# Kernel tuning notes

Hardware: AMD Instinct MI355X
Metric: run time of the kernel (lower is better)

The kernel has to match this reference:

```python
import jax, jax.numpy as jnp
import numpy as np

N_HEAD = 16
R = 4  # reciprocal rank

def setup_inputs() -> dict:
    key = jax.random.key(0)
    ks = jax.random.split(key, 8)
    B, T, C = 2, 2048, 1024
    H = N_HEAD
    D = C // H
    D_std = D - R
    x = jax.random.normal(ks[0], (B, T, C), dtype=jnp.float32)
    W_attn = jax.random.normal(ks[1], (3 * C, C), dtype=jnp.float32) * (1.0 / np.sqrt(C))
    W_proj = jax.random.normal(ks[2], (C, C), dtype=jnp.float32) * (1.0 / np.sqrt(C))
    w_std = jnp.full((H,), D_std / D, dtype=jnp.float32)
    w_rec = jnp.full((H,), R / D, dtype=jnp.float32)
    skip_std = jnp.float32(2.0)
    skip_low = jnp.float32(-3.0)
    rwr_alpha = jnp.full((H,), 0.05, dtype=jnp.float32)
    return {"x": x, "W_attn": W_attn, "W_proj": W_proj, "w_std": w_std,
            "w_rec": w_rec, "skip_std": skip_std, "skip_low": skip_low,
            "rwr_alpha": rwr_alpha}

def reference(x, W_attn, W_proj, w_std, w_rec, skip_std, skip_low, rwr_alpha):
    B, T, C = x.shape
    H = N_HEAD
    D = C // H
    D_std = D - R
    # fused QKV projection: [Qf | Kf | V]
    fused = jnp.einsum('btc,fc->btf', x, W_attn)
    qf, kf, v = jnp.split(fused, 3, axis=-1)
    Qf = qf.reshape(B, T, H, D).transpose(0, 2, 1, 3)  # (B,H,T,D)
    Kf = kf.reshape(B, T, H, D).transpose(0, 2, 1, 3)
    V = v.reshape(B, T, H, D).transpose(0, 2, 1, 3)
    # dynamic per-head gate scaling folded into Qf/Kf
    g_std = jnp.sqrt(jnp.clip(w_std * jax.nn.sigmoid(skip_std), 1e-8))  # (H,)
    g_rec = jnp.sqrt(jnp.clip(w_rec * jax.nn.sigmoid(skip_low), 1e-8))  # (H,)
    scale = jnp.concatenate([
        jnp.broadcast_to(g_std[:, None], (H, D_std)),
        jnp.broadcast_to(g_rec[:, None], (H, R)),
    ], axis=-1)  # (H, D)
    scale = scale[None, :, None, :]  # (1,H,1,D)
    Qf = Qf * scale
    Kf = Kf * scale
    # causal SDPA (scale = 1/sqrt(head_dim), dropout=0)
    scores = jnp.einsum('bhqd,bhkd->bhqk', Qf, Kf) / jnp.sqrt(jnp.float32(D))
    causal = jnp.tril(jnp.ones((T, T), dtype=bool))
    scores = jnp.where(causal[None, None], scores, jnp.float32(-1e30))
    attn = jax.nn.softmax(scores, axis=-1)
    y = jnp.einsum('bhqk,bhkd->bhqd', attn, V)
    # self-restart mix: out = (1-alpha)*attn_out + alpha*V, alpha in [0, 0.5]
    alpha = jnp.clip(rwr_alpha, 0.0, 0.5)[None, :, None, None]
    y = (1.0 - alpha) * y + alpha * V
    y = y.transpose(0, 2, 1, 3).reshape(B, T, C)
    return jnp.einsum('btc,oc->bto', y, W_proj)
```

## Files before the change

kernel.cpp:

```cpp
#include <hip/hip_runtime.h>
#include <hip/hip_bf16.h>
#include <math.h>
#include <stdint.h>

#define B_    2
#define T_    2048
#define C_    1024
#define H_    16
#define D_    64
#define R_    4
#define DSTD  60
#define F_    3072
#define BT_   (B_ * T_)

#define LOG2E 1.44269504088896340736f

typedef __bf16 bf16x8 __attribute__((ext_vector_type(8)));
typedef __bf16 bf16x4 __attribute__((ext_vector_type(4)));
typedef float  f32x4  __attribute__((ext_vector_type(4)));

__device__ __forceinline__ int swz(int row, int blk) {
    return blk ^ ((row >> 1) & 7);
}

__device__ __forceinline__ void st_pair(__bf16* p, __bf16 a, __bf16 b) {
    union { __bf16 h[2]; uint32_t u; } t;
    t.h[0] = a; t.h[1] = b;
    *(uint32_t*)p = t.u;
}

__device__ __forceinline__ void gload_lds16(const void* g, void* l) {
    __builtin_amdgcn_global_load_lds(
        (const __attribute__((address_space(1))) uint32_t*)g,
        (__attribute__((address_space(3))) uint32_t*)l, 16, 0, 0);
}

__global__ __launch_bounds__(256) void cast3_kernel(
    const float* __restrict__ a, int na4,
    const float* __restrict__ b, int nb4,
    const float* __restrict__ c, int nc4,
    __bf16* __restrict__ oa, __bf16* __restrict__ ob, __bf16* __restrict__ oc)
{
    int i = blockIdx.x * 256 + threadIdx.x;
    const float* s; __bf16* d; int j = i;
    if (j < na4) { s = a; d = oa; }
    else {
        j -= na4;
        if (j < nb4) { s = b; d = ob; }
        else {
            j -= nb4;
            if (j >= nc4) return;
            s = c; d = oc;
        }
    }
    float4 v = ((const float4*)s)[j];
    bf16x4 o;
    o[0] = (__bf16)v.x; o[1] = (__bf16)v.y;
    o[2] = (__bf16)v.z; o[3] = (__bf16)v.w;
    ((bf16x4*)d)[j] = o;
}

__global__ __launch_bounds__(256) void gemm_qkv_kernel(
    const __bf16* __restrict__ A,
    const __bf16* __restrict__ Bw,
    const float* __restrict__ w_std, const float* __restrict__ w_rec,
    const float* __restrict__ skip_std, const float* __restrict__ skip_low,
    __bf16* __restrict__ Q, __bf16* __restrict__ K, __bf16* __restrict__ V)
{
    __shared__ __bf16 As[128 * 64];
    __shared__ __bf16 Bs[128 * 64];

    const int tid  = threadIdx.x;
    const int row0 = blockIdx.x * 128;
    const int col0 = blockIdx.y * 128;

    const int w    = tid >> 6;
    const int lane = tid & 63;
    const int quad = lane >> 4;
    const int lt   = lane & 15;
    const int wm   = w >> 1;
    const int wn   = w & 1;

    const int srow = tid >> 3;
    const int sblk = tid & 7;

    f32x4 acc[4][4];
#pragma unroll
    for (int i = 0; i < 4; ++i)
#pragma unroll
        for (int j = 0; j < 4; ++j)
#pragma unroll
            for (int r = 0; r < 4; ++r) acc[i][j][r] = 0.f;

    for (int kt = 0; kt < C_ / 64; ++kt) {
        const int k0 = kt * 64;
        __syncthreads();
#pragma unroll
        for (int cc = 0; cc < 4; ++cc) {
            const int r  = cc * 32 + srow;
            const int sb = sblk ^ ((r >> 1) & 7);
            gload_lds16(A  + (size_t)(row0 + r) * C_ + k0 + sb * 8,
                        As + cc * 2048 + tid * 8);
            gload_lds16(Bw + (size_t)(col0 + r) * C_ + k0 + sb * 8,
                        Bs + cc * 2048 + tid * 8);
        }
        __syncthreads();

        bf16x8 waf[2][4], xf[2][4];
#pragma unroll
        for (int kk = 0; kk < 2; ++kk)
#pragma unroll
            for (int i = 0; i < 4; ++i) {
                const int rf = wn * 64 + i * 16 + lt;
                waf[kk][i] = *(const bf16x8*)&Bs[rf * 64 + swz(rf, kk * 4 + quad) * 8];
                const int rt = wm * 64 + i * 16 + lt;
                xf[kk][i]  = *(const bf16x8*)&As[rt * 64 + swz(rt, kk * 4 + quad) * 8];
            }
#pragma unroll
        for (int kk = 0; kk < 2; ++kk)
#pragma unroll
            for (int i = 0; i < 4; ++i)
#pragma unroll
                for (int j = 0; j < 4; ++j)
                    acc[i][j] = __builtin_amdgcn_mfma_f32_16x16x32_bf16(
                        waf[kk][i], xf[kk][j], acc[i][j], 0, 0, 0);
    }

    const int colbase = col0 + wn * 64;
    const int which   = colbase >> 10;
    const int h       = (colbase & (C_ - 1)) >> 6;

    const float ss = 1.f / (1.f + __expf(-skip_std[0]));
    const float sl = 1.f / (1.f + __expf(-skip_low[0]));
    const float gs = sqrtf(fmaxf(w_std[h] * ss, 1e-8f));
    const float gr = sqrtf(fmaxf(w_rec[h] * sl, 1e-8f));

    __bf16* dstM = (which == 0) ? Q : (which == 1) ? K : V;

#pragma unroll
    for (int i = 0; i < 4; ++i) {
        const int d0 = i * 16 + quad * 4;
        float sc = (d0 < DSTD) ? gs : gr;
        if (which == 0) sc *= 0.125f * LOG2E;
        const bool scale = (which != 2);
#pragma unroll
        for (int j = 0; j < 4; ++j) {
            const int trow = row0 + wm * 64 + j * 16 + lt;
            const int b = trow >> 11;
            const int t = trow & (T_ - 1);
            bf16x4 o;
#pragma unroll
            for (int r = 0; r < 4; ++r) {
                float v = acc[i][j][r];
                if (scale) v *= sc;
                o[r] = (__bf16)v;
            }
            *(bf16x4*)(dstM + (((size_t)b * H_ + h) * T_ + t) * D_ + d0) = o;
        }
    }
}

__global__ __launch_bounds__(256) void gemm_out_kernel(
    const __bf16* __restrict__ A,
    const __bf16* __restrict__ Bw,
    float* __restrict__ out)
{
    __shared__ __bf16 As[128 * 32];
    __shared__ __bf16 Bs[64 * 32];

    const int tid  = threadIdx.x;
    const int row0 = blockIdx.x * 128;
    const int col0 = blockIdx.y * 64;

    const int w    = tid >> 6;
    const int lane = tid & 63;
    const int quad = lane >> 4;
    const int lt   = lane & 15;
    const int wm   = w >> 1;
    const int wn   = w & 1;

    const int lrow = tid >> 2;
    const int lcol = (tid & 3) * 8;
    const int brow = tid >> 2;
    const int bcol = (tid & 3) * 8;

    f32x4 acc[2][4];
#pragma unroll
    for (int i = 0; i < 2; ++i)
#pragma unroll
        for (int j = 0; j < 4; ++j)
#pragma unroll
            for (int r = 0; r < 4; ++r) acc[i][j][r] = 0.f;

    for (int kt = 0; kt < C_ / 32; ++kt) {
        const int k0 = kt * 32;
        __syncthreads();
#pragma unroll
        for (int rr = 0; rr < 2; ++rr)
            gload_lds16(A + (size_t)(row0 + rr * 64 + lrow) * C_ + k0 + lcol,
                        As + rr * 2048 + tid * 8);
        gload_lds16(Bw + (size_t)(col0 + brow) * C_ + k0 + bcol,
                    Bs + tid * 8);
        __syncthreads();

        bf16x8 wpf[2], yf[4];
#pragma unroll
        for (int i = 0; i < 2; ++i)
            wpf[i] = *(const bf16x8*)&Bs[(wn * 32 + i * 16 + lt) * 32 + quad * 8];
#pragma unroll
        for (int j = 0; j < 4; ++j)
            yf[j] = *(const bf16x8*)&As[(wm * 64 + j * 16 + lt) * 32 + quad * 8];
#pragma unroll
        for (int i = 0; i < 2; ++i)
#pragma unroll
            for (int j = 0; j < 4; ++j)
                acc[i][j] = __builtin_amdgcn_mfma_f32_16x16x32_bf16(
                    wpf[i], yf[j], acc[i][j], 0, 0, 0);
    }

#pragma unroll
    for (int i = 0; i < 2; ++i) {
        const int o = col0 + wn * 32 + i * 16 + quad * 4;
#pragma unroll
        for (int j = 0; j < 4; ++j) {
            const int trow = row0 + wm * 64 + j * 16 + lt;
            float4 v;
            v.x = acc[i][j][0]; v.y = acc[i][j][1];
            v.z = acc[i][j][2]; v.w = acc[i][j][3];
            *(float4*)(out + (size_t)trow * C_ + o) = v;
        }
    }
}

__global__ __launch_bounds__(256) void attn_kernel(
    const __bf16* __restrict__ Q, const __bf16* __restrict__ K,
    const __bf16* __restrict__ V, const float* __restrict__ rwr_alpha,
    __bf16* __restrict__ Y)
{
    __shared__ __align__(16) __bf16 Ks[2][64][64];
    __shared__ __align__(16) __bf16 Vt[2][64][64];
    __shared__ __align__(16) __bf16 Ps[4][16][64];

    const int tid = threadIdx.x;
    const int bh  = blockIdx.x & 31;
    const int g   = blockIdx.x >> 5;
    const int qt  = (g < 8) ? (31 - g) : (g < 16) ? (g - 8)
                  : (g < 24) ? (39 - g) : (g - 16);
    const int h   = bh & (H_ - 1);
    const int b   = bh >> 4;

    const __bf16* Qb = Q + (((size_t)b * H_ + h) * T_) * D_;
    const __bf16* Kb = K + (((size_t)b * H_ + h) * T_) * D_;
    const __bf16* Vb = V + (((size_t)b * H_ + h) * T_) * D_;

    const int w    = tid >> 6;
    const int lane = tid & 63;
    const int quad = lane >> 4;
    const int lt   = lane & 15;

    const int kr0 = tid >> 3;
    const int kc0 = (tid & 7) ^ ((kr0 >> 1) & 7);
    const int kr1 = 32 + kr0;
    const int kc1 = (tid & 7) ^ ((kr1 >> 1) & 7);

    const int kp = (tid >> 3) * 2;
    const int dc = (tid & 7) * 8;
    const int kblk = kp >> 3, koff = kp & 7;

    const __bf16* qrow = Qb + (size_t)(qt * 64 + w * 16 + lt) * D_;
    bf16x8 qf[2];
    qf[0] = *(const bf16x8*)(qrow + quad * 8);
    qf[1] = *(const bf16x8*)(qrow + 32 + quad * 8);

    bf16x8 ones;
#pragma unroll
    for (int u = 0; u < 8; ++u) ones[u] = (__bf16)1.0f;

    gload_lds16(Kb + (size_t)kr0 * 64 + kc0 * 8, &Ks[0][0][0] + tid * 8);
    gload_lds16(Kb + (size_t)kr1 * 64 + kc1 * 8, &Ks[0][32][0] + tid * 8);
    {
        const __bf16* vs = Vb + (size_t)kp * 64 + dc;
        bf16x8 v1 = *(const bf16x8*)(vs);
        bf16x8 v2 = *(const bf16x8*)(vs + 64);
#pragma unroll
        for (int u = 0; u < 8; ++u) {
            const int row = dc + u;
            st_pair(&Vt[0][row][swz(row, kblk) * 8 + koff], v1[u], v2[u]);
        }
    }
    __syncthreads();

    f32x4 lacc;
    f32x4 oacc[4];
#pragma unroll
    for (int r = 0; r < 4; ++r) lacc[r] = 0.f;
#pragma unroll
    for (int n = 0; n < 4; ++n)
#pragma unroll
        for (int r = 0; r < 4; ++r) oacc[n][r] = 0.f;

    for (int kt = 0; kt <= qt; ++kt) {
        const int cur = kt & 1;
        const int nxt = 1 - cur;
        const bool pre = (kt < qt);

        bf16x8 v1, v2;
        if (pre) {
            const size_t toff = (size_t)(kt + 1) * 4096;
            gload_lds16(Kb + toff + (size_t)kr0 * 64 + kc0 * 8, &Ks[nxt][0][0] + tid * 8);
            gload_lds16(Kb + toff + (size_t)kr1 * 64 + kc1 * 8, &Ks[nxt][32][0] + tid * 8);
            const __bf16* vs = Vb + toff + (size_t)kp * 64 + dc;
            v1 = *(const bf16x8*)(vs);
            v2 = *(const bf16x8*)(vs + 64);
        }

        f32x4 sacc[4];
#pragma unroll
        for (int n = 0; n < 4; ++n)
#pragma unroll
            for (int r = 0; r < 4; ++r) sacc[n][r] = 0.f;
#pragma unroll
        for (int kk = 0; kk < 2; ++kk) {
#pragma unroll
            for (int n = 0; n < 4; ++n) {
                const int row = n * 16 + lt;
                bf16x8 ak = *(const bf16x8*)&Ks[cur][row][swz(row, kk * 4 + quad) * 8];
                sacc[n] = __builtin_amdgcn_mfma_f32_16x16x32_bf16(ak, qf[kk], sacc[n], 0, 0, 0);
            }
        }

        if (kt == qt) {
            const int ql = w * 16 + lt;
#pragma unroll
            for (int n = 0; n < 4; ++n) {
                const int keyb = n * 16 + quad * 4;
#pragma unroll
                for (int r = 0; r < 4; ++r)
                    if (keyb + r > ql) sacc[n][r] = -1e30f;
            }
        }

#pragma unroll
        for (int n = 0; n < 4; ++n) {
            bf16x4 pv;
#pragma unroll
            for (int r = 0; r < 4; ++r)
                pv[r] = (__bf16)__builtin_amdgcn_exp2f(sacc[n][r]);
            *(bf16x4*)&Ps[w][lt][swz(lt, n * 2 + (quad >> 1)) * 8 + (quad & 1) * 4] = pv;
        }

#pragma unroll
        for (int kk = 0; kk < 2; ++kk) {
            bf16x8 ap = *(const bf16x8*)&Ps[w][lt][swz(lt, kk * 4 + quad) * 8];
            lacc = __builtin_amdgcn_mfma_f32_16x16x32_bf16(ap, ones, lacc, 0, 0, 0);
#pragma unroll
            for (int nd = 0; nd < 4; ++nd) {
                const int drow = nd * 16 + lt;
                bf16x8 bv = *(const bf16x8*)&Vt[cur][drow][swz(drow, kk * 4 + quad) * 8];
                oacc[nd] = __builtin_amdgcn_mfma_f32_16x16x32_bf16(ap, bv, oacc[nd], 0, 0, 0);
            }
        }

        {
            const float lm = fmaxf(fmaxf(lacc[0], lacc[1]), fmaxf(lacc[2], lacc[3]));
            if (__ballot(lm > 1.0e12f)) {
                const float sc = 1.0f / 4294967296.0f;
#pragma unroll
                for (int r = 0; r < 4; ++r) lacc[r] *= sc;
#pragma unroll
                for (int n = 0; n < 4; ++n)
#pragma unroll
                    for (int r = 0; r < 4; ++r) oacc[n][r] *= sc;
            }
        }

        if (pre) {
#pragma unroll
            for (int u = 0; u < 8; ++u) {
                const int row = dc + u;
                st_pair(&Vt[nxt][row][swz(row, kblk) * 8 + koff], v1[u], v2[u]);
            }
        }
        __syncthreads();
    }

    const float a = fminf(fmaxf(rwr_alpha[h], 0.f), 0.5f);
#pragma unroll
    for (int r = 0; r < 4; ++r) {
        const float inv = 1.f / lacc[r];
        const int qg = qt * 64 + w * 16 + quad * 4 + r;
        const __bf16* vp = Vb + (size_t)qg * D_;
        __bf16* yp = Y + ((size_t)(b * T_ + qg)) * C_ + h * D_;
#pragma unroll
        for (int nd = 0; nd < 4; ++nd) {
            const int d = nd * 16 + lt;
            yp[d] = (__bf16)((1.f - a) * oacc[nd][r] * inv + a * (float)vp[d]);
        }
    }
}

extern "C" void kernel_launch(void* const* d_in, const int* in_sizes, int n_in,
                              void* d_out, int out_size, void* d_ws, size_t ws_size,
                              hipStream_t stream) {
    const float* x        = (const float*)d_in[0];
    const float* W_attn   = (const float*)d_in[1];
    const float* W_proj   = (const float*)d_in[2];
    const float* w_std    = (const float*)d_in[3];
    const float* w_rec    = (const float*)d_in[4];
    const float* skip_std = (const float*)d_in[5];
    const float* skip_low = (const float*)d_in[6];
    const float* rwr      = (const float*)d_in[7];
    float* out = (float*)d_out;

    const size_t nX  = (size_t)BT_ * C_;
    const size_t nWa = (size_t)F_ * C_;
    const size_t nWp = (size_t)C_ * C_;
    const size_t per = (size_t)B_ * H_ * T_ * D_;

    __bf16* xb  = (__bf16*)d_ws;
    __bf16* Wab = xb  + nX;
    __bf16* Wpb = Wab + nWa;
    __bf16* Qb  = Wpb + nWp;
    __bf16* Kb  = Qb  + per;
    __bf16* Vb  = Kb  + per;
    __bf16* Yb  = Vb  + per;

    const int na4 = nX / 4, nb4 = nWa / 4, nc4 = nWp / 4;
    cast3_kernel<<<dim3((na4 + nb4 + nc4 + 255) / 256), 256, 0, stream>>>(
        x, na4, W_attn, nb4, W_proj, nc4, xb, Wab, Wpb);

    gemm_qkv_kernel<<<dim3(BT_ / 128, F_ / 128), 256, 0, stream>>>(
        xb, Wab, w_std, w_rec, skip_std, skip_low, Qb, Kb, Vb);
    attn_kernel<<<dim3(32 * (T_ / 64)), 256, 0, stream>>>(Qb, Kb, Vb, rwr, Yb);
    gemm_out_kernel<<<dim3(BT_ / 128, C_ / 64), 256, 0, stream>>>(Yb, Wpb, out);
}
```

Measured before the change: 179.4 us.

## Double-buffer GEMM LDS tiles and load attention K directly from global

Both GEMM kernels now use double-buffered LDS tiles with BK=32, prefetching the next k-tile while computing the current one, which cuts barriers to one per iteration. The QKV GEMM drops its swizzled 64-wide tiles for unswizzled 32-wide tiles, which may add LDS bank conflicts. The attention kernel no longer stages K in shared memory; each wave reads its K fragments straight from global memory (L2/L1). That lowers LDS use but makes the four waves load K redundantly and exposes global latency inside the loop.

```diff
diff --git a/kernel.cpp b/kernel.cpp
--- a/kernel.cpp
+++ b/kernel.cpp
@@ -67,8 +67,8 @@
     const float* __restrict__ skip_std, const float* __restrict__ skip_low,
     __bf16* __restrict__ Q, __bf16* __restrict__ K, __bf16* __restrict__ V)
 {
-    __shared__ __bf16 As[128 * 64];
-    __shared__ __bf16 Bs[128 * 64];
+    __shared__ __bf16 As[2][128 * 32];
+    __shared__ __bf16 Bs[2][128 * 32];
 
     const int tid  = threadIdx.x;
     const int row0 = blockIdx.x * 128;
@@ -81,8 +81,8 @@
     const int wm   = w >> 1;
     const int wn   = w & 1;
 
-    const int srow = tid >> 3;
-    const int sblk = tid & 7;
+    const int lrow = tid >> 2;
+    const int lcol = (tid & 3) * 8;
 
     f32x4 acc[4][4];
 #pragma unroll
@@ -92,38 +92,41 @@
 #pragma unroll
             for (int r = 0; r < 4; ++r) acc[i][j][r] = 0.f;
 
-    for (int kt = 0; kt < C_ / 64; ++kt) {
-        const int k0 = kt * 64;
+#pragma unroll
+    for (int rr = 0; rr < 2; ++rr) {
+        gload_lds16(A  + (size_t)(row0 + rr * 64 + lrow) * C_ + lcol,
+                    &As[0][rr * 2048 + tid * 8]);
+        gload_lds16(Bw + (size_t)(col0 + rr * 64 + lrow) * C_ + lcol,
+                    &Bs[0][rr * 2048 + tid * 8]);
+    }
+    __syncthreads();
+
+    for (int kt = 0; kt < 32; ++kt) {
+        const int cur = kt & 1;
+        if (kt < 31) {
+            const int k0 = (kt + 1) * 32;
+#pragma unroll
+            for (int rr = 0; rr < 2; ++rr) {
+                gload_lds16(A  + (size_t)(row0 + rr * 64 + lrow) * C_ + k0 + lcol,
+                            &As[cur ^ 1][rr * 2048 + tid * 8]);
+                gload_lds16(Bw + (size_t)(col0 + rr * 64 + lrow) * C_ + k0 + lcol,
+                            &Bs[cur ^ 1][rr * 2048 + tid * 8]);
+            }
+        }
+
+        bf16x8 waf[4], xf[4];
+#pragma unroll
+        for (int i = 0; i < 4; ++i) {
+            waf[i] = *(const bf16x8*)&Bs[cur][(wn * 64 + i * 16 + lt) * 32 + quad * 8];
+            xf[i]  = *(const bf16x8*)&As[cur][(wm * 64 + i * 16 + lt) * 32 + quad * 8];
+        }
+#pragma unroll
+        for (int i = 0; i < 4; ++i)
+#pragma unroll
+            for (int j = 0; j < 4; ++j)
+                acc[i][j] = __builtin_amdgcn_mfma_f32_16x16x32_bf16(
+                    waf[i], xf[j], acc[i][j], 0, 0, 0);
         __syncthreads();
-#pragma unroll
-        for (int cc = 0; cc < 4; ++cc) {
-            const int r  = cc * 32 + srow;
-            const int sb = sblk ^ ((r >> 1) & 7);
-            gload_lds16(A  + (size_t)(row0 + r) * C_ + k0 + sb * 8,
-                        As + cc * 2048 + tid * 8);
-            gload_lds16(Bw + (size_t)(col0 + r) * C_ + k0 + sb * 8,
-                        Bs + cc * 2048 + tid * 8);
-        }
-        __syncthreads();
-
-        bf16x8 waf[2][4], xf[2][4];
-#pragma unroll
-        for (int kk = 0; kk < 2; ++kk)
-#pragma unroll
-            for (int i = 0; i < 4; ++i) {
-                const int rf = wn * 64 + i * 16 + lt;
-                waf[kk][i] = *(const bf16x8*)&Bs[rf * 64 + swz(rf, kk * 4 + quad) * 8];
-                const int rt = wm * 64 + i * 16 + lt;
-                xf[kk][i]  = *(const bf16x8*)&As[rt * 64 + swz(rt, kk * 4 + quad) * 8];
-            }
-#pragma unroll
-        for (int kk = 0; kk < 2; ++kk)
-#pragma unroll
-            for (int i = 0; i < 4; ++i)
-#pragma unroll
-                for (int j = 0; j < 4; ++j)
-                    acc[i][j] = __builtin_amdgcn_mfma_f32_16x16x32_bf16(
-                        waf[kk][i], xf[kk][j], acc[i][j], 0, 0, 0);
     }
 
     const int colbase = col0 + wn * 64;
@@ -165,8 +168,8 @@
     const __bf16* __restrict__ Bw,
     float* __restrict__ out)
 {
-    __shared__ __bf16 As[128 * 32];
-    __shared__ __bf16 Bs[64 * 32];
+    __shared__ __bf16 As[2][128 * 32];
+    __shared__ __bf16 Bs[2][64 * 32];
 
     const int tid  = threadIdx.x;
     const int row0 = blockIdx.x * 128;
@@ -181,8 +184,6 @@
 
     const int lrow = tid >> 2;
     const int lcol = (tid & 3) * 8;
-    const int brow = tid >> 2;
-    const int bcol = (tid & 3) * 8;
 
     f32x4 acc[2][4];
 #pragma unroll
@@ -192,30 +193,39 @@
 #pragma unroll
             for (int r = 0; r < 4; ++r) acc[i][j][r] = 0.f;
 
-    for (int kt = 0; kt < C_ / 32; ++kt) {
-        const int k0 = kt * 32;
-        __syncthreads();
-#pragma unroll
-        for (int rr = 0; rr < 2; ++rr)
-            gload_lds16(A + (size_t)(row0 + rr * 64 + lrow) * C_ + k0 + lcol,
-                        As + rr * 2048 + tid * 8);
-        gload_lds16(Bw + (size_t)(col0 + brow) * C_ + k0 + bcol,
-                    Bs + tid * 8);
-        __syncthreads();
+#pragma unroll
+    for (int rr = 0; rr < 2; ++rr)
+        gload_lds16(A + (size_t)(row0 + rr * 64 + lrow) * C_ + lcol,
+                    &As[0][rr * 2048 + tid * 8]);
+    gload_lds16(Bw + (size_t)(col0 + lrow) * C_ + lcol, &Bs[0][tid * 8]);
+    __syncthreads();
+
+    for (int kt = 0; kt < 32; ++kt) {
+        const int cur = kt & 1;
+        if (kt < 31) {
+            const int k0 = (kt + 1) * 32;
+#pragma unroll
+            for (int rr = 0; rr < 2; ++rr)
+                gload_lds16(A + (size_t)(row0 + rr * 64 + lrow) * C_ + k0 + lcol,
+                            &As[cur ^ 1][rr * 2048 + tid * 8]);
+            gload_lds16(Bw + (size_t)(col0 + lrow) * C_ + k0 + lcol,
+                        &Bs[cur ^ 1][tid * 8]);
+        }
 
         bf16x8 wpf[2], yf[4];
 #pragma unroll
         for (int i = 0; i < 2; ++i)
-            wpf[i] = *(const bf16x8*)&Bs[(wn * 32 + i * 16 + lt) * 32 + quad * 8];
+            wpf[i] = *(const bf16x8*)&Bs[cur][(wn * 32 + i * 16 + lt) * 32 + quad * 8];
 #pragma unroll
         for (int j = 0; j < 4; ++j)
-            yf[j] = *(const bf16x8*)&As[(wm * 64 + j * 16 + lt) * 32 + quad * 8];
+            yf[j] = *(const bf16x8*)&As[cur][(wm * 64 + j * 16 + lt) * 32 + quad * 8];
 #pragma unroll
         for (int i = 0; i < 2; ++i)
 #pragma unroll
             for (int j = 0; j < 4; ++j)
                 acc[i][j] = __builtin_amdgcn_mfma_f32_16x16x32_bf16(
                     wpf[i], yf[j], acc[i][j], 0, 0, 0);
+        __syncthreads();
     }
 
 #pragma unroll
@@ -237,7 +247,6 @@
     const __bf16* __restrict__ V, const float* __restrict__ rwr_alpha,
     __bf16* __restrict__ Y)
 {
-    __shared__ __align__(16) __bf16 Ks[2][64][64];
     __shared__ __align__(16) __bf16 Vt[2][64][64];
     __shared__ __align__(16) __bf16 Ps[4][16][64];
 
@@ -258,11 +267,6 @@
     const int quad = lane >> 4;
     const int lt   = lane & 15;
 
-    const int kr0 = tid >> 3;
-    const int kc0 = (tid & 7) ^ ((kr0 >> 1) & 7);
-    const int kr1 = 32 + kr0;
-    const int kc1 = (tid & 7) ^ ((kr1 >> 1) & 7);
-
     const int kp = (tid >> 3) * 2;
     const int dc = (tid & 7) * 8;
     const int kblk = kp >> 3, koff = kp & 7;
@@ -276,8 +280,6 @@
 #pragma unroll
     for (int u = 0; u < 8; ++u) ones[u] = (__bf16)1.0f;
 
-    gload_lds16(Kb + (size_t)kr0 * 64 + kc0 * 8, &Ks[0][0][0] + tid * 8);
-    gload_lds16(Kb + (size_t)kr1 * 64 + kc1 * 8, &Ks[0][32][0] + tid * 8);
     {
         const __bf16* vs = Vb + (size_t)kp * 64 + dc;
         bf16x8 v1 = *(const bf16x8*)(vs);
@@ -306,28 +308,31 @@
 
         bf16x8 v1, v2;
         if (pre) {
-            const size_t toff = (size_t)(kt + 1) * 4096;
-            gload_lds16(Kb + toff + (size_t)kr0 * 64 + kc0 * 8, &Ks[nxt][0][0] + tid * 8);
-            gload_lds16(Kb + toff + (size_t)kr1 * 64 + kc1 * 8, &Ks[nxt][32][0] + tid * 8);
-            const __bf16* vs = Vb + toff + (size_t)kp * 64 + dc;
+            const __bf16* vs = Vb + (size_t)(kt + 1) * 4096 + (size_t)kp * 64 + dc;
             v1 = *(const bf16x8*)(vs);
             v2 = *(const bf16x8*)(vs + 64);
         }
 
+        const __bf16* kb_t = Kb + (size_t)kt * 4096;
+        bf16x8 akf[2][4];
+#pragma unroll
+        for (int kk = 0; kk < 2; ++kk)
+#pragma unroll
+            for (int n = 0; n < 4; ++n)
+                akf[kk][n] = *(const bf16x8*)(kb_t + (size_t)(n * 16 + lt) * 64
+                                              + kk * 32 + quad * 8);
+
         f32x4 sacc[4];
 #pragma unroll
         for (int n = 0; n < 4; ++n)
 #pragma unroll
             for (int r = 0; r < 4; ++r) sacc[n][r] = 0.f;
 #pragma unroll
-        for (int kk = 0; kk < 2; ++kk) {
-#pragma unroll
-            for (int n = 0; n < 4; ++n) {
-                const int row = n * 16 + lt;
-                bf16x8 ak = *(const bf16x8*)&Ks[cur][row][swz(row, kk * 4 + quad) * 8];
-                sacc[n] = __builtin_amdgcn_mfma_f32_16x16x32_bf16(ak, qf[kk], sacc[n], 0, 0, 0);
-            }
-        }
+        for (int kk = 0; kk < 2; ++kk)
+#pragma unroll
+            for (int n = 0; n < 4; ++n)
+                sacc[n] = __builtin_amdgcn_mfma_f32_16x16x32_bf16(
+                    akf[kk][n], qf[kk], sacc[n], 0, 0, 0);
 
         if (kt == qt) {
             const int ql = w * 16 + lt;
```

New measurement: 227.2 us. 1.27x slower.
